# Kernel tuning notes

Hardware: AMD Instinct MI355X
Metric: run time of the kernel (lower is better)

## Reference

```python
import jax, jax.numpy as jnp
import numpy as np

# Dims matching init_kwargs
T = 2048          # tokens in sentence
M = 6144          # total morphemes (ragged, ~3 per token)
WV = 200000       # word2vec vocab
EMB = 100         # word2vec dim (LSTMINPDIM == TOKDIM == 100)
DP_V = 50         # dp vocab
DPDIM = 64
FEAT = 36
HID = 128         # HIDDENDIM//2 per direction
TAGS = 50
IN0 = 2 * EMB + DPDIM + FEAT   # 300, input to LSTM layer 0
IN1 = 2 * HID                  # 256, input to LSTM layer 1


def setup_inputs() -> dict:
    key = jax.random.key(0)
    ks = jax.random.split(key, 24)
    s = 0.02
    inp = {
        "morp_ids": jax.random.randint(ks[0], (M,), 0, WV),
        "segment_ids": jnp.sort(jax.random.randint(ks[1], (M,), 0, T)),
        "pred_idx": 100,
        "dp_in": jax.random.randint(ks[2], (T,), 0, DP_V),
        "feat_vector": jax.random.uniform(ks[3], (T, FEAT), dtype=jnp.float32),
        # parameters
        "W_wv": jax.random.normal(ks[4], (WV, EMB), dtype=jnp.float32) * s,
        "dp_table": jax.random.normal(ks[5], (DP_V, DPDIM), dtype=jnp.float32) * s,
        "W_out": jax.random.normal(ks[6], (TAGS, 2 * HID), dtype=jnp.float32) * s,
        "b_out": jnp.zeros((TAGS,), dtype=jnp.float32),
    }
    i = 7
    for l, in_dim in ((0, IN0), (1, IN1)):
        for d in ("f", "b"):
            inp[f"w_ih_l{l}{d}"] = jax.random.normal(ks[i], (4 * HID, in_dim), dtype=jnp.float32) * s; i += 1
            inp[f"w_hh_l{l}{d}"] = jax.random.normal(ks[i], (4 * HID, HID), dtype=jnp.float32) * s; i += 1
            inp[f"b_l{l}{d}"] = jnp.zeros((4 * HID,), dtype=jnp.float32)  # b_ih + b_hh combined
    return inp


def _lstm_dir(x, w_ih, w_hh, b, reverse):
    # x: [T, in_dim] (batch of 1 squeezed). torch gate order: i, f, g, o.
    xp = x @ w_ih.T + b                      # [T, 4H]
    if reverse:
        xp = xp[::-1]
    H = w_hh.shape[1]
    h0 = jnp.zeros((H,), dtype=x.dtype)
    c0 = jnp.zeros((H,), dtype=x.dtype)

    def step(carry, g_t):
        h, c = carry
        g = g_t + h @ w_hh.T                 # [4H]
        i, f, gg, o = jnp.split(g, 4)
        i, f, o = jax.nn.sigmoid(i), jax.nn.sigmoid(f), jax.nn.sigmoid(o)
        c = f * c + i * jnp.tanh(gg)
        h = o * jnp.tanh(c)
        return (h, c), h

    _, hs = jax.lax.scan(step, (h0, c0), xp)  # [T, H]
    return hs[::-1] if reverse else hs


def _bilstm_layer(x, w_ih_f, w_hh_f, b_f, w_ih_b, w_hh_b, b_b):
    hf = _lstm_dir(x, w_ih_f, w_hh_f, b_f, reverse=False)
    hb = _lstm_dir(x, w_ih_b, w_hh_b, b_b, reverse=True)
    return jnp.concatenate([hf, hb], axis=-1)  # [T, 2H]


def reference(morp_ids, segment_ids, pred_idx, dp_in, feat_vector,
              W_wv, dp_table, W_out, b_out,
              w_ih_l0f, w_hh_l0f, b_l0f, w_ih_l0b, w_hh_l0b, b_l0b,
              w_ih_l1f, w_hh_l1f, b_l1f, w_ih_l1b, w_hh_l1b, b_l1b):
    # Fused embedding-bag: gather morpheme vectors, segment-sum per token.
    morp_vecs = W_wv[morp_ids]                                   # [M, EMB]
    tok_sums = jax.ops.segment_sum(morp_vecs, segment_ids, num_segments=T)  # [T, EMB]
    pred_vec = tok_sums[pred_idx]                                # [EMB]
    tok_vec = jnp.concatenate([tok_sums, jnp.broadcast_to(pred_vec, (T, EMB))], axis=1)  # [T, 2*EMB]
    dp_embs = dp_table[dp_in]                                    # [T, DPDIM]
    inp = jnp.concatenate([tok_vec, dp_embs, feat_vector], axis=1)  # [T, IN0]
    h1 = _bilstm_layer(inp, w_ih_l0f, w_hh_l0f, b_l0f, w_ih_l0b, w_hh_l0b, b_l0b)
    h2 = _bilstm_layer(h1, w_ih_l1f, w_hh_l1f, b_l1f, w_ih_l1b, w_hh_l1b, b_l1b)
    tag_space = h2 @ W_out.T + b_out                             # [T, TAGS]
    return tag_space
```

## Files before the change

### kernel.cpp

```cpp
#include <hip/hip_runtime.h>

#define T_SEQ 2048
#define NMORPH 6144
#define EMB 100
#define HID 128
#define GATES 512
#define LDA0 304
#define XPD 1024
#define TAGS 50

typedef float  fx4 __attribute__((ext_vector_type(4)));
typedef unsigned int ux4 __attribute__((ext_vector_type(4)));

__device__ __forceinline__ float sigm(float x) {
  return 1.0f / (1.0f + __expf(-x));
}
__device__ __forceinline__ float tanh_f(float x) {
  x = fminf(fmaxf(x, -9.0f), 9.0f);
  float e2 = __expf(2.0f * x);
  return (e2 - 1.0f) / (e2 + 1.0f);
}
__device__ __forceinline__ unsigned int f2bf1(float x) {
  unsigned int u = __float_as_uint(x);
  return (u + 0x7FFFu + ((u >> 16) & 1u)) >> 16;
}
__device__ __forceinline__ float bf2f(unsigned int h) {
  return __uint_as_float(h << 16);
}
__device__ __forceinline__ unsigned int pack2(float a, float b) {
  return f2bf1(a) | (f2bf1(b) << 16);
}
__device__ __forceinline__ float lof(float x) {
  return x - bf2f(f2bf1(x));
}

__global__ void k_toksum(const float* __restrict__ W_wv,
                         const int* __restrict__ morp_ids,
                         const int* __restrict__ seg,
                         float* __restrict__ inp) {
  const int t = blockIdx.x;
  const int d = threadIdx.x;
  int a = 0, b = NMORPH;
  while (a < b) { int m = (a + b) >> 1; if (seg[m] < t) a = m + 1; else b = m; }
  const int lo = a;
  b = NMORPH;
  while (a < b) { int m = (a + b) >> 1; if (seg[m] <= t) a = m + 1; else b = m; }
  const int hi = a;
  if (d < EMB) {
    float s = 0.0f;
    for (int m = lo; m < hi; ++m)
      s += W_wv[(size_t)morp_ids[m] * EMB + d];
    inp[(size_t)t * LDA0 + d] = s;
  }
}

__global__ void k_fill(const float* __restrict__ dp_table,
                       const int* __restrict__ dp_in,
                       const float* __restrict__ feat,
                       const int* __restrict__ pred_idx,
                       float* __restrict__ inp) {
  const int t = blockIdx.x;
  const int c = threadIdx.x;
  if (c >= 204) return;
  const int col = 100 + c;
  float v;
  if (col < 200)      v = inp[(size_t)pred_idx[0] * LDA0 + (col - 100)];
  else if (col < 264) v = dp_table[dp_in[t] * 64 + (col - 200)];
  else if (col < 300) v = feat[t * 36 + (col - 264)];
  else                v = 0.0f;
  inp[(size_t)t * LDA0 + col] = v;
}

__global__ __launch_bounds__(256) void k_gemm(
    const float* __restrict__ A, int lda, int K,
    const float* __restrict__ Wf, const float* __restrict__ Wb,
    const float* __restrict__ bf, const float* __restrict__ bb,
    float* __restrict__ out) {
  constexpr int BK = 16, LDT = 68;
  __shared__ float As[BK][LDT];
  __shared__ float Bs[BK][LDT];
  const int tid = threadIdx.x;
  const int tx = tid & 15, ty = tid >> 4;
  const int bm = blockIdx.x * 64;
  const int n0 = blockIdx.y * 64;
  const float* __restrict__ W  = (n0 < GATES) ? Wf : Wb;
  const float* __restrict__ bs = (n0 < GATES) ? bf : bb;
  const int nw = (n0 < GATES) ? n0 : n0 - GATES;
  const int ar = tid >> 2;
  const int ak = (tid & 3) * 4;
  float acc[4][4] = {};
  const int ktiles = (K + BK - 1) / BK;
  for (int kt = 0; kt < ktiles; ++kt) {
    const int k0 = kt * BK;
    float4 av = *(const float4*)&A[(size_t)(bm + ar) * lda + k0 + ak];
    float4 bv = make_float4(0.f, 0.f, 0.f, 0.f);
    if (k0 + ak < K)
      bv = *(const float4*)&W[(size_t)(nw + ar) * K + k0 + ak];
    __syncthreads();
    As[ak + 0][ar] = av.x; As[ak + 1][ar] = av.y;
    As[ak + 2][ar] = av.z; As[ak + 3][ar] = av.w;
    Bs[ak + 0][ar] = bv.x; Bs[ak + 1][ar] = bv.y;
    Bs[ak + 2][ar] = bv.z; Bs[ak + 3][ar] = bv.w;
    __syncthreads();
#pragma unroll
    for (int kk = 0; kk < BK; ++kk) {
      float4 a4 = *(const float4*)&As[kk][ty * 4];
      float4 b4 = *(const float4*)&Bs[kk][tx * 4];
      float a_[4] = {a4.x, a4.y, a4.z, a4.w};
      float b_[4] = {b4.x, b4.y, b4.z, b4.w};
#pragma unroll
      for (int i = 0; i < 4; ++i)
#pragma unroll
        for (int j = 0; j < 4; ++j)
          acc[i][j] = fmaf(a_[i], b_[j], acc[i][j]);
    }
  }
  const float4 bias4 = *(const float4*)&bs[nw + tx * 4];
#pragma unroll
  for (int i = 0; i < 4; ++i) {
    float4 o;
    o.x = acc[i][0] + bias4.x;
    o.y = acc[i][1] + bias4.y;
    o.z = acc[i][2] + bias4.z;
    o.w = acc[i][3] + bias4.w;
    *(float4*)&out[(size_t)(bm + ty * 4 + i) * XPD + n0 + tx * 4] = o;
  }
}

#define STASH4(A0, A1, A2, A3, V)                                  \
  asm volatile("v_accvgpr_write_b32 " A0 ", %0\n\t"                \
               "v_accvgpr_write_b32 " A1 ", %1\n\t"                \
               "v_accvgpr_write_b32 " A2 ", %2\n\t"                \
               "v_accvgpr_write_b32 " A3 ", %3"                    \
               :: "v"(V[0]), "v"(V[1]), "v"(V[2]), "v"(V[3])       \
               : A0, A1, A2, A3)

#define FRAG(TN, KC, H0,H1,H2,H3, L0,L1,L2,L3)                     \
  do {                                                             \
    const float* wp_ = whh + (size_t)(wbase + (TN)*16 + ln15)*HID  \
                       + (KC)*32 + kg8;                            \
    float4 f0_ = *(const float4*)wp_;                              \
    float4 f1_ = *(const float4*)(wp_ + 4);                        \
    ux4 H_, L_;                                                    \
    H_[0] = pack2(f0_.x, f0_.y);  H_[1] = pack2(f0_.z, f0_.w);     \
    H_[2] = pack2(f1_.x, f1_.y);  H_[3] = pack2(f1_.z, f1_.w);     \
    L_[0] = pack2(lof(f0_.x), lof(f0_.y));                         \
    L_[1] = pack2(lof(f0_.z), lof(f0_.w));                         \
    L_[2] = pack2(lof(f1_.x), lof(f1_.y));                         \
    L_[3] = pack2(lof(f1_.z), lof(f1_.w));                         \
    STASH4(H0, H1, H2, H3, H_);                                    \
    STASH4(L0, L1, L2, L3, L_);                                    \
  } while (0)

#define MFMA4(ACC, AV, AR)                                         \
  asm volatile("v_mfma_f32_16x16x32_bf16 %0, %1, " AR ", %0"       \
               : "+v"(ACC) : "v"(AV))

#define ACLOB                                                       \
  "a0","a1","a2","a3","a4","a5","a6","a7","a8","a9","a10","a11",    \
  "a12","a13","a14","a15","a16","a17","a18","a19","a20","a21",      \
  "a22","a23","a24","a25","a26","a27","a28","a29","a30","a31",      \
  "a32","a33","a34","a35","a36","a37","a38","a39","a40","a41",      \
  "a42","a43","a44","a45","a46","a47","a48","a49","a50","a51",      \
  "a52","a53","a54","a55","a56","a57","a58","a59","a60","a61",      \
  "a62","a63","a64","a65","a66","a67","a68","a69","a70","a71",      \
  "a72","a73","a74","a75","a76","a77","a78","a79","a80","a81",      \
  "a82","a83","a84","a85","a86","a87","a88","a89","a90","a91",      \
  "a92","a93","a94","a95","a96","a97","a98","a99","a100","a101",    \
  "a102","a103","a104","a105","a106","a107","a108","a109","a110",   \
  "a111","a112","a113","a114","a115","a116","a117","a118","a119",   \
  "a120","a121","a122","a123","a124","a125","a126","a127"

__global__ __launch_bounds__(512) void k_lstm(
    const float* __restrict__ xp,
    const float* __restrict__ whh_f,
    const float* __restrict__ whh_b,
    float* __restrict__ hout) {
  const int dir = blockIdx.x;
  const int tid = threadIdx.x;
  const int wv  = tid >> 6;
  const int ln  = tid & 63;
  const int ln15 = ln & 15;
  const int kg8  = (ln >> 4) * 8;
  const int wbase = wv * 64;
  const float* __restrict__ whh = dir ? whh_b : whh_f;
  const int xofs = dir * GATES;
  const int hofs = dir * HID;

  __shared__ __align__(16) float lx[2 * 8 * GATES];
  __shared__ __align__(16) float lg[GATES];
  __shared__ __align__(16) unsigned short hbf[2][2][136];

  FRAG(0, 0, "a0","a1","a2","a3",     "a64","a65","a66","a67");
  FRAG(0, 1, "a4","a5","a6","a7",     "a68","a69","a70","a71");
  FRAG(0, 2, "a8","a9","a10","a11",   "a72","a73","a74","a75");
  FRAG(0, 3, "a12","a13","a14","a15", "a76","a77","a78","a79");
  FRAG(1, 0, "a16","a17","a18","a19", "a80","a81","a82","a83");
  FRAG(1, 1, "a20","a21","a22","a23", "a84","a85","a86","a87");
  FRAG(1, 2, "a24","a25","a26","a27", "a88","a89","a90","a91");
  FRAG(1, 3, "a28","a29","a30","a31", "a92","a93","a94","a95");
  FRAG(2, 0, "a32","a33","a34","a35", "a96","a97","a98","a99");
  FRAG(2, 1, "a36","a37","a38","a39", "a100","a101","a102","a103");
  FRAG(2, 2, "a40","a41","a42","a43", "a104","a105","a106","a107");
  FRAG(2, 3, "a44","a45","a46","a47", "a108","a109","a110","a111");
  FRAG(3, 0, "a48","a49","a50","a51", "a112","a113","a114","a115");
  FRAG(3, 1, "a52","a53","a54","a55", "a116","a117","a118","a119");
  FRAG(3, 2, "a56","a57","a58","a59", "a120","a121","a122","a123");
  FRAG(3, 3, "a60","a61","a62","a63", "a124","a125","a126","a127");

  const int xu = tid >> 6;
  const int xc = (tid & 63) * 8;
  {
    const int tt = dir ? (T_SEQ - 1 - xu) : xu;
    const float* gp = xp + (size_t)tt * XPD + xofs + xc;
    *(fx4*)&lx[tid * 8]     = *(const fx4*)gp;
    *(fx4*)&lx[tid * 8 + 4] = *(const fx4*)(gp + 4);
  }
  float c = 0.0f;
  if (tid < HID) {
    hbf[0][0][tid] = 0; hbf[0][1][tid] = 0;
  }
  __syncthreads();

  int buf = 0;
  for (int t0 = 0; t0 < T_SEQ; t0 += 8) {
    const int tb = (t0 + 8 < T_SEQ) ? t0 + 8 : 0;
    fx4 xr0, xr1;
    {
      const int tg = tb + xu;
      const int tt = dir ? (T_SEQ - 1 - tg) : tg;
      const float* gp = xp + (size_t)tt * XPD + xofs + xc;
      asm volatile("global_load_dwordx4 %0, %2, off\n\t"
                   "global_load_dwordx4 %1, %2, off offset:16"
                   : "=&v"(xr0), "=&v"(xr1) : "v"(gp));
    }
    const float* lxb = lx + buf * (8 * GATES);
#pragma unroll
    for (int u = 0; u < 8; ++u) {
      const int t = t0 + u;
      const int tt = dir ? (T_SEQ - 1 - t) : t;
      const int p = t & 1;
      const unsigned short* ap = (ln15 == 1 ? &hbf[p][1][0] : &hbf[p][0][0]) + kg8;
      ux4 av0 = *(const ux4*)(ap);
      ux4 av1 = *(const ux4*)(ap + 32);
      ux4 av2 = *(const ux4*)(ap + 64);
      ux4 av3 = *(const ux4*)(ap + 96);
      fx4 acc0 = {0.f, 0.f, 0.f, 0.f};
      fx4 acc1 = {0.f, 0.f, 0.f, 0.f};
      fx4 acc2 = {0.f, 0.f, 0.f, 0.f};
      fx4 acc3 = {0.f, 0.f, 0.f, 0.f};
      asm volatile("s_nop 1"
                   : "+v"(acc0), "+v"(acc1), "+v"(acc2), "+v"(acc3)
                   :: ACLOB);
      MFMA4(acc0, av0, "a[0:3]");
      MFMA4(acc1, av0, "a[16:19]");
      MFMA4(acc2, av0, "a[32:35]");
      MFMA4(acc3, av0, "a[48:51]");
      MFMA4(acc0, av1, "a[4:7]");
      MFMA4(acc1, av1, "a[20:23]");
      MFMA4(acc2, av1, "a[36:39]");
      MFMA4(acc3, av1, "a[52:55]");
      MFMA4(acc0, av2, "a[8:11]");
      MFMA4(acc1, av2, "a[24:27]");
      MFMA4(acc2, av2, "a[40:43]");
      MFMA4(acc3, av2, "a[56:59]");
      MFMA4(acc0, av3, "a[12:15]");
      MFMA4(acc1, av3, "a[28:31]");
      MFMA4(acc2, av3, "a[44:47]");
      MFMA4(acc3, av3, "a[60:63]");
      MFMA4(acc0, av0, "a[64:67]");
      MFMA4(acc1, av0, "a[80:83]");
      MFMA4(acc2, av0, "a[96:99]");
      MFMA4(acc3, av0, "a[112:115]");
      MFMA4(acc0, av1, "a[68:71]");
      MFMA4(acc1, av1, "a[84:87]");
      MFMA4(acc2, av1, "a[100:103]");
      MFMA4(acc3, av1, "a[116:119]");
      MFMA4(acc0, av2, "a[72:75]");
      MFMA4(acc1, av2, "a[88:91]");
      MFMA4(acc2, av2, "a[104:107]");
      MFMA4(acc3, av2, "a[120:123]");
      MFMA4(acc0, av3, "a[76:79]");
      MFMA4(acc1, av3, "a[92:95]");
      MFMA4(acc2, av3, "a[108:111]");
      MFMA4(acc3, av3, "a[124:127]");
      asm volatile("s_nop 7\n\ts_nop 7\n\ts_nop 7"
                   : "+v"(acc0), "+v"(acc1), "+v"(acc2), "+v"(acc3));
      float g0 = acc0[0] + acc0[1] + lxb[u * GATES + wbase +  0 + ln15];
      float g1 = acc1[0] + acc1[1] + lxb[u * GATES + wbase + 16 + ln15];
      float g2 = acc2[0] + acc2[1] + lxb[u * GATES + wbase + 32 + ln15];
      float g3 = acc3[0] + acc3[1] + lxb[u * GATES + wbase + 48 + ln15];
      const int cls = wv >> 1;
      float a0, a1, a2, a3;
      if (cls == 2) {
        a0 = tanh_f(g0); a1 = tanh_f(g1); a2 = tanh_f(g2); a3 = tanh_f(g3);
      } else {
        a0 = sigm(g0);   a1 = sigm(g1);   a2 = sigm(g2);   a3 = sigm(g3);
      }
      if (ln < 16) {
        lg[wbase +  0 + ln] = a0;
        lg[wbase + 16 + ln] = a1;
        lg[wbase + 32 + ln] = a2;
        lg[wbase + 48 + ln] = a3;
      }
      asm volatile("s_waitcnt lgkmcnt(0)" ::: "memory");
      __builtin_amdgcn_s_barrier();
      if (tid < HID) {
        float gi = lg[tid];
        float gf = lg[HID + tid];
        float gg = lg[2 * HID + tid];
        float go = lg[3 * HID + tid];
        c = gf * c + gi * gg;
        float h = go * tanh_f(c);
        unsigned int hh = f2bf1(h);
        float hr = h - bf2f(hh);
        hbf[p ^ 1][0][tid] = (unsigned short)hh;
        hbf[p ^ 1][1][tid] = (unsigned short)f2bf1(hr);
        hout[(size_t)tt * 256 + hofs + tid] = h;
      }
      if (u == 7) {
        asm volatile("s_waitcnt vmcnt(0)" ::: "memory");
        *(fx4*)&lx[(buf ^ 1) * (8 * GATES) + tid * 8]     = xr0;
        *(fx4*)&lx[(buf ^ 1) * (8 * GATES) + tid * 8 + 4] = xr1;
      }
      asm volatile("s_waitcnt lgkmcnt(0)" ::: "memory");
      __builtin_amdgcn_s_barrier();
    }
    buf ^= 1;
  }
}

__global__ void k_out(const float* __restrict__ h2,
                      const float* __restrict__ Wout,
                      const float* __restrict__ bout,
                      float* __restrict__ out) {
  __shared__ __align__(16) float hrow[256];
  const int t = blockIdx.x;
  const int tid = threadIdx.x;
  *(float4*)&hrow[tid * 4] = *(const float4*)&h2[(size_t)t * 256 + tid * 4];
  __syncthreads();
  if (tid < TAGS) {
    float acc = bout[tid];
    const float* w = &Wout[(size_t)tid * 256];
#pragma unroll 8
    for (int k = 0; k < 256; k += 4) {
      float4 wv = *(const float4*)&w[k];
      acc += hrow[k] * wv.x + hrow[k + 1] * wv.y + hrow[k + 2] * wv.z +
             hrow[k + 3] * wv.w;
    }
    out[(size_t)t * TAGS + tid] = acc;
  }
}

extern "C" void kernel_launch(void* const* d_in, const int* in_sizes, int n_in,
                              void* d_out, int out_size, void* d_ws, size_t ws_size,
                              hipStream_t stream) {
  const int*   morp_ids = (const int*)d_in[0];
  const int*   seg      = (const int*)d_in[1];
  const int*   pred_idx = (const int*)d_in[2];
  const int*   dp_in    = (const int*)d_in[3];
  const float* feat     = (const float*)d_in[4];
  const float* W_wv     = (const float*)d_in[5];
  const float* dp_table = (const float*)d_in[6];
  const float* W_out    = (const float*)d_in[7];
  const float* b_out    = (const float*)d_in[8];
  const float* w_ih_l0f = (const float*)d_in[9];
  const float* w_hh_l0f = (const float*)d_in[10];
  const float* b_l0f    = (const float*)d_in[11];
  const float* w_ih_l0b = (const float*)d_in[12];
  const float* w_hh_l0b = (const float*)d_in[13];
  const float* b_l0b    = (const float*)d_in[14];
  const float* w_ih_l1f = (const float*)d_in[15];
  const float* w_hh_l1f = (const float*)d_in[16];
  const float* b_l1f    = (const float*)d_in[17];
  const float* w_ih_l1b = (const float*)d_in[18];
  const float* w_hh_l1b = (const float*)d_in[19];
  const float* b_l1b    = (const float*)d_in[20];
  float* out = (float*)d_out;

  float* ws  = (float*)d_ws;
  float* inp = ws;
  float* xp  = inp + 2048 * LDA0;
  float* h1  = xp + 2048 * XPD;
  float* h2  = h1 + 2048 * 256;

  k_toksum<<<2048, 128, 0, stream>>>(W_wv, morp_ids, seg, inp);
  k_fill<<<2048, 256, 0, stream>>>(dp_table, dp_in, feat, pred_idx, inp);

  dim3 gg(32, 16);
  k_gemm<<<gg, 256, 0, stream>>>(inp, LDA0, 300, w_ih_l0f, w_ih_l0b, b_l0f, b_l0b, xp);
  k_lstm<<<2, 512, 0, stream>>>(xp, w_hh_l0f, w_hh_l0b, h1);
  k_gemm<<<gg, 256, 0, stream>>>(h1, 256, 256, w_ih_l1f, w_ih_l1b, b_l1f, b_l1b, xp);
  k_lstm<<<2, 512, 0, stream>>>(xp, w_hh_l1f, w_hh_l1b, h2);
  k_out<<<2048, 64, 0, stream>>>(h2, W_out, b_out, out);
}
```

Before: 4.037 ms.

## Remap LSTM gate rows per wave so each wave owns whole hidden units

Reassigns W_hh rows so each wave holds the i, f, g, o rows for the same 16 hidden units. The cell update can then run inside the wave without the shared gate buffer and one of the two barriers per timestep. The precomputed input projection is injected as the MFMA accumulator's initial value. The hi and lo MFMA chains are split into separate accumulators to shorten dependency chains. The cell state is now computed redundantly across lanes, and correctness depends on the new row mapping matching the accumulator lane layout.

```diff
diff --git a/kernel.cpp b/kernel.cpp
--- a/kernel.cpp
+++ b/kernel.cpp
@@ -137,7 +137,7 @@
 
 #define FRAG(TN, KC, H0,H1,H2,H3, L0,L1,L2,L3)                     \
   do {                                                             \
-    const float* wp_ = whh + (size_t)(wbase + (TN)*16 + ln15)*HID  \
+    const float* wp_ = whh + (size_t)((TN)*128 + wtile + ln15)*HID \
                        + (KC)*32 + kg8;                            \
     float4 f0_ = *(const float4*)wp_;                              \
     float4 f1_ = *(const float4*)(wp_ + 4);                        \
@@ -182,13 +182,12 @@
   const int ln  = tid & 63;
   const int ln15 = ln & 15;
   const int kg8  = (ln >> 4) * 8;
-  const int wbase = wv * 64;
+  const int wtile = wv * 16;
   const float* __restrict__ whh = dir ? whh_b : whh_f;
   const int xofs = dir * GATES;
   const int hofs = dir * HID;
 
   __shared__ __align__(16) float lx[2 * 8 * GATES];
-  __shared__ __align__(16) float lg[GATES];
   __shared__ __align__(16) unsigned short hbf[2][2][136];
 
   FRAG(0, 0, "a0","a1","a2","a3",     "a64","a65","a66","a67");
@@ -220,6 +219,12 @@
   if (tid < HID) {
     hbf[0][0][tid] = 0; hbf[0][1][tid] = 0;
   }
+  float* hp = hout + (size_t)(dir ? (T_SEQ - 1) : 0) * 256 + hofs + wtile + ln15;
+  const ptrdiff_t hstep = dir ? -256 : 256;
+
+  fx4 ah0 = {0,0,0,0}, ah1 = {0,0,0,0}, ah2 = {0,0,0,0}, ah3 = {0,0,0,0};
+  fx4 al0 = {0,0,0,0}, al1 = {0,0,0,0}, al2 = {0,0,0,0}, al3 = {0,0,0,0};
+
   __syncthreads();
 
   int buf = 0;
@@ -237,87 +242,79 @@
     const float* lxb = lx + buf * (8 * GATES);
 #pragma unroll
     for (int u = 0; u < 8; ++u) {
-      const int t = t0 + u;
-      const int tt = dir ? (T_SEQ - 1 - t) : t;
-      const int p = t & 1;
-      const unsigned short* ap = (ln15 == 1 ? &hbf[p][1][0] : &hbf[p][0][0]) + kg8;
+      const int p = u & 1;
+      const float* xrow = lxb + u * GATES + wtile + ln15;
+      float x_i = xrow[0];
+      float x_f = xrow[128];
+      float x_g = xrow[256];
+      float x_o = xrow[384];
+      const unsigned short* ap =
+          (ln15 == 1 ? &hbf[p][1][0] : &hbf[p][0][0]) + kg8;
       ux4 av0 = *(const ux4*)(ap);
       ux4 av1 = *(const ux4*)(ap + 32);
       ux4 av2 = *(const ux4*)(ap + 64);
       ux4 av3 = *(const ux4*)(ap + 96);
-      fx4 acc0 = {0.f, 0.f, 0.f, 0.f};
-      fx4 acc1 = {0.f, 0.f, 0.f, 0.f};
-      fx4 acc2 = {0.f, 0.f, 0.f, 0.f};
-      fx4 acc3 = {0.f, 0.f, 0.f, 0.f};
+      ah0[0] = x_i; ah0[1] = 0.f;
+      ah1[0] = x_f; ah1[1] = 0.f;
+      ah2[0] = x_g; ah2[1] = 0.f;
+      ah3[0] = x_o; ah3[1] = 0.f;
+      al0[0] = 0.f; al0[1] = 0.f;
+      al1[0] = 0.f; al1[1] = 0.f;
+      al2[0] = 0.f; al2[1] = 0.f;
+      al3[0] = 0.f; al3[1] = 0.f;
       asm volatile("s_nop 1"
-                   : "+v"(acc0), "+v"(acc1), "+v"(acc2), "+v"(acc3)
+                   : "+v"(ah0), "+v"(ah1), "+v"(ah2), "+v"(ah3),
+                     "+v"(al0), "+v"(al1), "+v"(al2), "+v"(al3)
                    :: ACLOB);
-      MFMA4(acc0, av0, "a[0:3]");
-      MFMA4(acc1, av0, "a[16:19]");
-      MFMA4(acc2, av0, "a[32:35]");
-      MFMA4(acc3, av0, "a[48:51]");
-      MFMA4(acc0, av1, "a[4:7]");
-      MFMA4(acc1, av1, "a[20:23]");
-      MFMA4(acc2, av1, "a[36:39]");
-      MFMA4(acc3, av1, "a[52:55]");
-      MFMA4(acc0, av2, "a[8:11]");
-      MFMA4(acc1, av2, "a[24:27]");
-      MFMA4(acc2, av2, "a[40:43]");
-      MFMA4(acc3, av2, "a[56:59]");
-      MFMA4(acc0, av3, "a[12:15]");
-      MFMA4(acc1, av3, "a[28:31]");
-      MFMA4(acc2, av3, "a[44:47]");
-      MFMA4(acc3, av3, "a[60:63]");
-      MFMA4(acc0, av0, "a[64:67]");
-      MFMA4(acc1, av0, "a[80:83]");
-      MFMA4(acc2, av0, "a[96:99]");
-      MFMA4(acc3, av0, "a[112:115]");
-      MFMA4(acc0, av1, "a[68:71]");
-      MFMA4(acc1, av1, "a[84:87]");
-      MFMA4(acc2, av1, "a[100:103]");
-      MFMA4(acc3, av1, "a[116:119]");
-      MFMA4(acc0, av2, "a[72:75]");
-      MFMA4(acc1, av2, "a[88:91]");
-      MFMA4(acc2, av2, "a[104:107]");
-      MFMA4(acc3, av2, "a[120:123]");
-      MFMA4(acc0, av3, "a[76:79]");
-      MFMA4(acc1, av3, "a[92:95]");
-      MFMA4(acc2, av3, "a[108:111]");
-      MFMA4(acc3, av3, "a[124:127]");
+      MFMA4(ah0, av0, "a[0:3]");
+      MFMA4(ah1, av0, "a[16:19]");
+      MFMA4(ah2, av0, "a[32:35]");
+      MFMA4(ah3, av0, "a[48:51]");
+      MFMA4(al0, av0, "a[64:67]");
+      MFMA4(al1, av0, "a[80:83]");
+      MFMA4(al2, av0, "a[96:99]");
+      MFMA4(al3, av0, "a[112:115]");
+      MFMA4(ah0, av1, "a[4:7]");
+      MFMA4(ah1, av1, "a[20:23]");
+      MFMA4(ah2, av1, "a[36:39]");
+      MFMA4(ah3, av1, "a[52:55]");
+      MFMA4(al0, av1, "a[68:71]");
+      MFMA4(al1, av1, "a[84:87]");
+      MFMA4(al2, av1, "a[100:103]");
+      MFMA4(al3, av1, "a[116:119]");
+      MFMA4(ah0, av2, "a[8:11]");
+      MFMA4(ah1, av2, "a[24:27]");
+      MFMA4(ah2, av2, "a[40:43]");
+      MFMA4(ah3, av2, "a[56:59]");
+      MFMA4(al0, av2, "a[72:75]");
+      MFMA4(al1, av2, "a[88:91]");
+      MFMA4(al2, av2, "a[104:107]");
+      MFMA4(al3, av2, "a[120:123]");
+      MFMA4(ah0, av3, "a[12:15]");
+      MFMA4(ah1, av3, "a[28:31]");
+      MFMA4(ah2, av3, "a[44:47]");
+      MFMA4(ah3, av3, "a[60:63]");
+      MFMA4(al0, av3, "a[76:79]");
+      MFMA4(al1, av3, "a[92:95]");
+      MFMA4(al2, av3, "a[108:111]");
+      MFMA4(al3, av3, "a[124:127]");
       asm volatile("s_nop 7\n\ts_nop 7\n\ts_nop 7"
-                   : "+v"(acc0), "+v"(acc1), "+v"(acc2), "+v"(acc3));
-      float g0 = acc0[0] + acc0[1] + lxb[u * GATES + wbase +  0 + ln15];
-      float g1 = acc1[0] + acc1[1] + lxb[u * GATES + wbase + 16 + ln15];
-      float g2 = acc2[0] + acc2[1] + lxb[u * GATES + wbase + 32 + ln15];
-      float g3 = acc3[0] + acc3[1] + lxb[u * GATES + wbase + 48 + ln15];
-      const int cls = wv >> 1;
-      float a0, a1, a2, a3;
-      if (cls == 2) {
-        a0 = tanh_f(g0); a1 = tanh_f(g1); a2 = tanh_f(g2); a3 = tanh_f(g3);
-      } else {
-        a0 = sigm(g0);   a1 = sigm(g1);   a2 = sigm(g2);   a3 = sigm(g3);
-      }
+                   : "+v"(ah0), "+v"(ah1), "+v"(ah2), "+v"(ah3),
+                     "+v"(al0), "+v"(al1), "+v"(al2), "+v"(al3));
+      float i_g = sigm(ah0[0] + ah0[1] + al0[0] + al0[1]);
+      float f_g = sigm(ah1[0] + ah1[1] + al1[0] + al1[1]);
+      float g_g = tanh_f(ah2[0] + ah2[1] + al2[0] + al2[1]);
+      float o_g = sigm(ah3[0] + ah3[1] + al3[0] + al3[1]);
+      c = f_g * c + i_g * g_g;
+      float h = o_g * tanh_f(c);
       if (ln < 16) {
-        lg[wbase +  0 + ln] = a0;
-        lg[wbase + 16 + ln] = a1;
-        lg[wbase + 32 + ln] = a2;
-        lg[wbase + 48 + ln] = a3;
-      }
-      asm volatile("s_waitcnt lgkmcnt(0)" ::: "memory");
-      __builtin_amdgcn_s_barrier();
-      if (tid < HID) {
-        float gi = lg[tid];
-        float gf = lg[HID + tid];
-        float gg = lg[2 * HID + tid];
-        float go = lg[3 * HID + tid];
-        c = gf * c + gi * gg;
-        float h = go * tanh_f(c);
         unsigned int hh = f2bf1(h);
         float hr = h - bf2f(hh);
-        hbf[p ^ 1][0][tid] = (unsigned short)hh;
-        hbf[p ^ 1][1][tid] = (unsigned short)f2bf1(hr);
-        hout[(size_t)tt * 256 + hofs + tid] = h;
+        hbf[p ^ 1][0][wtile + ln15] = (unsigned short)hh;
+        hbf[p ^ 1][1][wtile + ln15] = (unsigned short)f2bf1(hr);
+        *hp = h;
       }
+      hp += hstep;
       if (u == 7) {
         asm volatile("s_waitcnt vmcnt(0)" ::: "memory");
         *(fx4*)&lx[(buf ^ 1) * (8 * GATES) + tid * 8]     = xr0;
```

Measured after the change: 3.782 ms. -6.3%, faster.
